# Kernel optimization log

Measured on AMD Instinct MI355X. Metric: run time of the kernel, lower is better.

The kernel has to match this reference:

```python
import jax, jax.numpy as jnp
import numpy as np

N = 1024      # num_features
H = 256       # num_hidden_features
E = 64        # embedding_size
HD = 64       # hidden_size
B = 8192


def setup_inputs() -> dict:
    key = jax.random.key(0)
    ks = jax.random.split(key, 7)
    glorot_e = (2.0 / (N + E)) ** 0.5
    glorot_w = (2.0 / (2 * E + HD)) ** 0.5
    glorot_u = (2.0 / (HD + 1)) ** 0.5
    return {
        "values": jax.random.uniform(ks[0], (B, N), dtype=jnp.float32),
        "feat_emb": jax.random.normal(ks[1], (N, E), dtype=jnp.float32) * glorot_e,
        "hid_emb": jax.random.normal(ks[2], (H, E), dtype=jnp.float32) * glorot_e,
        "W_w": jax.random.normal(ks[3], (2 * E, HD), dtype=jnp.float32) * glorot_w,
        "b_w": jnp.zeros((HD,), dtype=jnp.float32),
        "W_u": jax.random.normal(ks[4], (HD, 1), dtype=jnp.float32) * glorot_u,
        "mask": jax.random.bernoulli(ks[5], 0.5, (N, N + H)),
    }


def _forward(values, feat_emb, hid_emb, W_w, b_w, W_u, mask):
    # full embedding table over extended vocab: [M, E], M = N + H
    full = jnp.concatenate([feat_emb, hid_emb], axis=0)
    # Dense w applied to concat([feat_i, full_j]) == split-matmul, avoids [N,M,2E]
    W1, W2 = W_w[:E], W_w[E:]                      # each [E, HD]
    a = feat_emb @ W1                              # [N, HD]
    b = full @ W2                                  # [M, HD]
    h = jnp.tanh(a[:, None, :] + b[None, :, :] + b_w)  # [N, M, HD]
    score = jnp.squeeze(h @ W_u, axis=-1)          # [N, M]
    score = jnp.where(mask, jnp.exp(score), 0.0)
    score_sum = jnp.sum(score, axis=1, keepdims=True)
    score_sum = jnp.where(score_sum == 0, 1.0, score_sum)
    attention_weights = score / score_sum          # [N, M]
    context = attention_weights @ full             # [N, E]
    return values @ context                        # [B, E]


def reference(values, feat_emb, hid_emb, W_w, b_w, W_u, mask):
    return _forward(values, feat_emb, hid_emb, W_w, b_w, W_u, mask)
```

## Files before the change

### kernel.cpp

```cpp
#include <hip/hip_runtime.h>
#include <hip/hip_bf16.h>

#define NF   1024
#define NHID 256
#define NJ   1280
#define ED   64
#define BATCH 8192

#define K2E   2.8853900817779268f
#define LOG2E 1.4426950408889634f

__device__ __forceinline__ float exp2_fast(float x) {
    float r;
    asm volatile("v_exp_f32 %0, %1" : "=v"(r) : "v"(x));
    return r;
}

__global__ __launch_bounds__(256) void prep_kernel(
    const float* __restrict__ feat, const float* __restrict__ hid,
    const float* __restrict__ Ww, const float* __restrict__ bw,
    float* __restrict__ Ap, float* __restrict__ BvT)
{
    __shared__ __align__(16) float in_s[64][64];
    __shared__ __align__(16) float tout[64][65];
    const int tid = threadIdx.x;
    const int b   = blockIdx.x;
    const bool isA = (b < 16);
    const int e  = tid & 63;
    const int wv = tid >> 6;

    const float* W = isA ? Ww : (Ww + 4096);
    float wcol[64];
    #pragma unroll
    for (int k = 0; k < 64; k++) wcol[k] = W[k * 64 + e];
    const float bias = isA ? 0.f : bw[e];

    const int bb = isA ? b : (b - 16);
    const float* src = isA ? (feat + (size_t)bb * 4096)
                     : (bb < 16 ? (feat + (size_t)bb * 4096)
                                : (hid + (size_t)(bb - 16) * 4096));
    #pragma unroll
    for (int s = 0; s < 4; s++)
        ((float4*)&in_s[0][0])[tid + s * 256] = ((const float4*)src)[tid + s * 256];
    __syncthreads();

    float acc[16];
    #pragma unroll
    for (int r = 0; r < 16; r++) acc[r] = bias;
    for (int k4 = 0; k4 < 64; k4 += 4) {
        #pragma unroll
        for (int r = 0; r < 16; r++) {
            float4 iv = *(const float4*)&in_s[wv * 16 + r][k4];
            acc[r] += iv.x*wcol[k4+0] + iv.y*wcol[k4+1] + iv.z*wcol[k4+2] + iv.w*wcol[k4+3];
        }
    }

    if (isA) {
        #pragma unroll
        for (int r = 0; r < 16; r++)
            Ap[(size_t)(b * 64 + wv * 16 + r) * 64 + e] = acc[r] * K2E;
    } else {
        #pragma unroll
        for (int r = 0; r < 16; r++) tout[wv * 16 + r][e] = acc[r] * K2E;
        __syncthreads();
        const int j0 = bb * 64;
        #pragma unroll
        for (int q = 0; q < 4; q++) {
            float4 v;
            v.x = tout[wv * 16 + q * 4 + 0][e];
            v.y = tout[wv * 16 + q * 4 + 1][e];
            v.z = tout[wv * 16 + q * 4 + 2][e];
            v.w = tout[wv * 16 + q * 4 + 3][e];
            *(float4*)&BvT[(size_t)e * NJ + j0 + wv * 16 + q * 4] = v;
        }
    }
}

__global__ __launch_bounds__(256) void score_kernel(
    const float* __restrict__ Wu, const float* __restrict__ Ap,
    const float* __restrict__ BvT, const void* __restrict__ maskp,
    float* __restrict__ sc)
{
    __shared__ __align__(16) float4 sA4[64];
    __shared__ float sWu2[64];
    __shared__ float sSwuL;
    __shared__ int   mtype_s;

    const int tid = threadIdx.x;
    const int iq  = blockIdx.x / 5;
    const int jc  = blockIdx.x - iq * 5;
    const int i0  = iq * 4;
    const int j   = jc * 256 + tid;

    if (tid < 64) {
        const unsigned int* mw = (const unsigned int*)maskp;
        unsigned int w = mw[tid];
        unsigned long long notf = __ballot(w != 0u && w != 0x3F800000u);
        unsigned long long gt1  = __ballot(w > 1u);
        if (tid == 0) mtype_s = (notf == 0ull) ? 2 : ((gt1 == 0ull) ? 1 : 0);
        float wu = Wu[tid];
        float4 p;
        p.x = Ap[(size_t)(i0 + 0) * 64 + tid];
        p.y = Ap[(size_t)(i0 + 1) * 64 + tid];
        p.z = Ap[(size_t)(i0 + 2) * 64 + tid];
        p.w = Ap[(size_t)(i0 + 3) * 64 + tid];
        sA4[tid]  = p;
        sWu2[tid] = wu * (2.0f * LOG2E);
        float s = wu;
        #pragma unroll
        for (int off = 32; off > 0; off >>= 1) s += __shfl_down(s, off);
        if (tid == 0) sSwuL = s * LOG2E;
    }
    __syncthreads();

    const float* bp = BvT + j;
    float acc0 = 0.f, acc1 = 0.f, acc2 = 0.f, acc3 = 0.f;
    #pragma unroll 8
    for (int e = 0; e < 64; e++) {
        float b  = bp[(size_t)e * NJ];
        float4 a = sA4[e];
        float w2 = sWu2[e];
        float t, r;
        t = a.x + b; r = __builtin_amdgcn_rcpf(exp2_fast(t) + 1.f); acc0 = fmaf(w2, r, acc0);
        t = a.y + b; r = __builtin_amdgcn_rcpf(exp2_fast(t) + 1.f); acc1 = fmaf(w2, r, acc1);
        t = a.z + b; r = __builtin_amdgcn_rcpf(exp2_fast(t) + 1.f); acc2 = fmaf(w2, r, acc2);
        t = a.w + b; r = __builtin_amdgcn_rcpf(exp2_fast(t) + 1.f); acc3 = fmaf(w2, r, acc3);
    }

    const float SwuL = sSwuL;
    const int mtype = mtype_s;
    const unsigned char* m8  = (const unsigned char*)maskp;
    const unsigned int*  m32 = (const unsigned int*)maskp;
    const float*         mfl = (const float*)maskp;
    float av[4] = {acc0, acc1, acc2, acc3};
    #pragma unroll
    for (int i = 0; i < 4; i++) {
        size_t off = (size_t)(i0 + i) * NJ + j;
        bool bm;
        if (mtype == 0)      bm = m8[off]  != 0;
        else if (mtype == 1) bm = m32[off] != 0u;
        else                 bm = mfl[off] != 0.f;
        sc[off] = bm ? exp2_fast(SwuL - av[i]) : 0.f;
    }
}

__global__ __launch_bounds__(256) void ctx_kernel(
    const float* __restrict__ feat, const float* __restrict__ hid,
    const float* __restrict__ sc, float* __restrict__ ctx)
{
    __shared__ __align__(16) float sc_s[4][NJ];
    __shared__ __align__(16) float red[4][16][64];
    __shared__ float ssum_s[4];
    const int tid = threadIdx.x;
    const int i0  = blockIdx.x * 4;

    #pragma unroll
    for (int rep = 0; rep < 5; rep++) {
        int idx = tid + rep * 256;
        int i   = idx / 320;
        int jq  = idx - i * 320;
        *(float4*)&sc_s[i][jq * 4] = *(const float4*)&sc[(size_t)(i0 + i) * NJ + jq * 4];
    }
    __syncthreads();
    {
        int i = tid >> 6, e = tid & 63;
        float s = 0.f;
        #pragma unroll
        for (int g = 0; g < 20; g++) s += sc_s[i][e + g * 64];
        #pragma unroll
        for (int off = 32; off > 0; off >>= 1) s += __shfl_down(s, off);
        if (e == 0) ssum_s[i] = (s == 0.f) ? 1.f : s;
    }

    const int jg = tid >> 4;
    const int e4 = (tid & 15) * 4;
    float4 c[4];
    #pragma unroll
    for (int i = 0; i < 4; i++) c[i] = make_float4(0.f, 0.f, 0.f, 0.f);
    for (int it = 0; it < 80; it++) {
        int j = it * 16 + jg;
        const float* fr = (j < NF) ? (feat + (size_t)j * 64)
                                   : (hid  + (size_t)(j - NF) * 64);
        float4 f = *(const float4*)(fr + e4);
        #pragma unroll
        for (int i = 0; i < 4; i++) {
            float w = sc_s[i][j];
            c[i].x += w*f.x; c[i].y += w*f.y; c[i].z += w*f.z; c[i].w += w*f.w;
        }
    }
    #pragma unroll
    for (int i = 0; i < 4; i++) *(float4*)&red[i][jg][e4] = c[i];
    __syncthreads();
    {
        int half = tid >> 6, e = tid & 63;
        float v = 0.f;
        #pragma unroll
        for (int g = 0; g < 16; g++) v += red[half][g][e];
        ctx[(size_t)(i0 + half) * 64 + e] = v / ssum_s[half];
    }
}

__global__ __launch_bounds__(256) void out_mm_kernel(
    const float* __restrict__ values, const float* __restrict__ ctxp,
    float* __restrict__ dst, int atomic_mode)
{
    __shared__ __align__(16) float vsT[64 * 64];
    __shared__ __align__(16) float cs[64][64];
    const int tid = threadIdx.x;
    const int rt  = blockIdx.x >> 3;
    const int kq  = blockIdx.x & 7;
    const int r0  = rt * 64;
    const int tr  = tid >> 4;
    const int tc4 = (tid & 15) * 4;

    float acc[4][4];
    #pragma unroll
    for (int a = 0; a < 4; a++)
        #pragma unroll
        for (int b = 0; b < 4; b++) acc[a][b] = 0.f;

    for (int ch = 0; ch < 2; ch++) {
        const int k0 = kq * 128 + ch * 64;
        __syncthreads();
        #pragma unroll
        for (int s = 0; s < 4; s++) {
            int t   = tid + s * 256;
            int r   = t >> 4;
            int kk4 = (t & 15) * 4;
            float4 g = *(const float4*)&values[(size_t)(r0 + r) * NF + k0 + kk4];
            int p  = (((r >> 2) + (t & 15)) & 15) * 4 + (r & 3);
            vsT[(kk4 + 0) * 64 + p] = g.x;
            vsT[(kk4 + 1) * 64 + p] = g.y;
            vsT[(kk4 + 2) * 64 + p] = g.z;
            vsT[(kk4 + 3) * 64 + p] = g.w;
        }
        #pragma unroll
        for (int s = 0; s < 4; s++) {
            int t  = tid + s * 256;
            int kk = t >> 4;
            int c4 = (t & 15) * 4;
            *(float4*)&cs[kk][c4] = *(const float4*)&ctxp[(size_t)(k0 + kk) * ED + c4];
        }
        __syncthreads();
        #pragma unroll 8
        for (int k = 0; k < 64; k++) {
            float4 av = *(const float4*)&vsT[k * 64 + (((tr + (k >> 2)) & 15) << 2)];
            float4 bv = *(const float4*)&cs[k][tc4];
            acc[0][0] += av.x*bv.x; acc[0][1] += av.x*bv.y; acc[0][2] += av.x*bv.z; acc[0][3] += av.x*bv.w;
            acc[1][0] += av.y*bv.x; acc[1][1] += av.y*bv.y; acc[1][2] += av.y*bv.z; acc[1][3] += av.y*bv.w;
            acc[2][0] += av.z*bv.x; acc[2][1] += av.z*bv.y; acc[2][2] += av.z*bv.z; acc[2][3] += av.z*bv.w;
            acc[3][0] += av.w*bv.x; acc[3][1] += av.w*bv.y; acc[3][2] += av.w*bv.z; acc[3][3] += av.w*bv.w;
        }
    }
    if (atomic_mode) {
        #pragma unroll
        for (int i2 = 0; i2 < 4; i2++) {
            int r = r0 + tr * 4 + i2;
            float* op = dst + (size_t)r * ED + tc4;
            unsafeAtomicAdd(op + 0, acc[i2][0]);
            unsafeAtomicAdd(op + 1, acc[i2][1]);
            unsafeAtomicAdd(op + 2, acc[i2][2]);
            unsafeAtomicAdd(op + 3, acc[i2][3]);
        }
    } else {
        #pragma unroll
        for (int i2 = 0; i2 < 4; i2++) {
            int r = r0 + tr * 4 + i2;
            float* op = dst + ((size_t)kq * BATCH + r) * ED + tc4;
            *(float4*)op = make_float4(acc[i2][0], acc[i2][1], acc[i2][2], acc[i2][3]);
        }
    }
}

__global__ __launch_bounds__(256) void reduce8_kernel(
    const float* __restrict__ part, float* __restrict__ out)
{
    const size_t S = (size_t)BATCH * ED / 4;
    size_t idx = (size_t)blockIdx.x * 256 + threadIdx.x;
    const float4* p = (const float4*)part;
    float4 r = {0.f, 0.f, 0.f, 0.f};
    #pragma unroll
    for (int q = 0; q < 8; q++) {
        float4 a = p[idx + (size_t)q * S];
        r.x += a.x; r.y += a.y; r.z += a.z; r.w += a.w;
    }
    ((float4*)out)[idx] = r;
}

extern "C" void kernel_launch(void* const* d_in, const int* in_sizes, int n_in,
                              void* d_out, int out_size, void* d_ws, size_t ws_size,
                              hipStream_t stream) {
    const float* values = (const float*)d_in[0];
    const float* feat   = (const float*)d_in[1];
    const float* hid    = (const float*)d_in[2];
    const float* Ww     = (const float*)d_in[3];
    const float* bw     = (const float*)d_in[4];
    const float* Wu     = (const float*)d_in[5];
    const void*  mask   = d_in[6];
    float* out = (float*)d_out;

    float* Ap  = (float*)d_ws;
    float* BvT = Ap + (size_t)NF * 64;
    float* ctx = BvT + (size_t)ED * NJ;
    float* sc  = ctx + (size_t)NF * 64;
    float* part = sc + (size_t)NF * NJ;
    const size_t need = ((size_t)NF*64 + (size_t)ED*NJ + (size_t)NF*64
                         + (size_t)NF*NJ + (size_t)8*BATCH*ED) * sizeof(float);
    const bool wsmode = ws_size >= need;

    hipLaunchKernelGGL(prep_kernel, dim3(36), dim3(256), 0, stream,
                       feat, hid, Ww, bw, Ap, BvT);
    hipLaunchKernelGGL(score_kernel, dim3(1280), dim3(256), 0, stream,
                       Wu, Ap, BvT, mask, sc);
    hipLaunchKernelGGL(ctx_kernel, dim3(256), dim3(256), 0, stream,
                       feat, hid, sc, ctx);
    if (wsmode) {
        hipLaunchKernelGGL(out_mm_kernel, dim3(1024), dim3(256), 0, stream,
                           values, ctx, part, 0);
        hipLaunchKernelGGL(reduce8_kernel, dim3(BATCH * ED / 4 / 256), dim3(256), 0, stream,
                           part, out);
    } else {
        hipMemsetAsync(d_out, 0, (size_t)BATCH * ED * sizeof(float), stream);
        hipLaunchKernelGGL(out_mm_kernel, dim3(1024), dim3(256), 0, stream,
                           values, ctx, out, 1);
    }
}
```

Before: 153.6 us.

## Move Wu reduction to prep, read A/Wu from global in score, halve ctx rows per block

Computes the Wu sum once in prep_kernel and stores it in workspace. score_kernel drops its shared-memory staging of A rows and scaled Wu, reading them directly from global/scalar memory (wave-uniform loads), and folds the 2*log2e scale into a final fma. ctx_kernel now handles 2 rows per block with 512 blocks for more parallelism, at the cost of reloading feature rows twice as often. The asm volatile on v_exp is relaxed to let the compiler schedule it.

```diff
diff --git a/kernel.cpp b/kernel.cpp
--- a/kernel.cpp
+++ b/kernel.cpp
@@ -12,14 +12,15 @@
 
 __device__ __forceinline__ float exp2_fast(float x) {
     float r;
-    asm volatile("v_exp_f32 %0, %1" : "=v"(r) : "v"(x));
+    asm("v_exp_f32 %0, %1" : "=v"(r) : "v"(x));
     return r;
 }
 
 __global__ __launch_bounds__(256) void prep_kernel(
     const float* __restrict__ feat, const float* __restrict__ hid,
     const float* __restrict__ Ww, const float* __restrict__ bw,
-    float* __restrict__ Ap, float* __restrict__ BvT)
+    const float* __restrict__ Wu,
+    float* __restrict__ Ap, float* __restrict__ BvT, float* __restrict__ swu)
 {
     __shared__ __align__(16) float in_s[64][64];
     __shared__ __align__(16) float tout[64][65];
@@ -29,6 +30,13 @@
     const int e  = tid & 63;
     const int wv = tid >> 6;
 
+    if (b == 0 && tid < 64) {
+        float s = Wu[tid];
+        #pragma unroll
+        for (int off = 32; off > 0; off >>= 1) s += __shfl_down(s, off);
+        if (tid == 0) swu[0] = s * LOG2E;
+    }
+
     const float* W = isA ? Ww : (Ww + 4096);
     float wcol[64];
     #pragma unroll
@@ -78,14 +86,10 @@
 
 __global__ __launch_bounds__(256) void score_kernel(
     const float* __restrict__ Wu, const float* __restrict__ Ap,
-    const float* __restrict__ BvT, const void* __restrict__ maskp,
-    float* __restrict__ sc)
-{
-    __shared__ __align__(16) float4 sA4[64];
-    __shared__ float sWu2[64];
-    __shared__ float sSwuL;
-    __shared__ int   mtype_s;
-
+    const float* __restrict__ BvT, const float* __restrict__ swu,
+    const void* __restrict__ maskp, float* __restrict__ sc)
+{
+    __shared__ int mtype_s;
     const int tid = threadIdx.x;
     const int iq  = blockIdx.x / 5;
     const int jc  = blockIdx.x - iq * 5;
@@ -98,36 +102,28 @@
         unsigned long long notf = __ballot(w != 0u && w != 0x3F800000u);
         unsigned long long gt1  = __ballot(w > 1u);
         if (tid == 0) mtype_s = (notf == 0ull) ? 2 : ((gt1 == 0ull) ? 1 : 0);
-        float wu = Wu[tid];
-        float4 p;
-        p.x = Ap[(size_t)(i0 + 0) * 64 + tid];
-        p.y = Ap[(size_t)(i0 + 1) * 64 + tid];
-        p.z = Ap[(size_t)(i0 + 2) * 64 + tid];
-        p.w = Ap[(size_t)(i0 + 3) * 64 + tid];
-        sA4[tid]  = p;
-        sWu2[tid] = wu * (2.0f * LOG2E);
-        float s = wu;
-        #pragma unroll
-        for (int off = 32; off > 0; off >>= 1) s += __shfl_down(s, off);
-        if (tid == 0) sSwuL = s * LOG2E;
     }
     __syncthreads();
 
-    const float* bp = BvT + j;
+    const float* a0p = Ap + (size_t)(i0 + 0) * 64;
+    const float* a1p = Ap + (size_t)(i0 + 1) * 64;
+    const float* a2p = Ap + (size_t)(i0 + 2) * 64;
+    const float* a3p = Ap + (size_t)(i0 + 3) * 64;
+    const float* bp  = BvT + j;
+
     float acc0 = 0.f, acc1 = 0.f, acc2 = 0.f, acc3 = 0.f;
     #pragma unroll 8
     for (int e = 0; e < 64; e++) {
         float b  = bp[(size_t)e * NJ];
-        float4 a = sA4[e];
-        float w2 = sWu2[e];
+        float wu = Wu[e];
         float t, r;
-        t = a.x + b; r = __builtin_amdgcn_rcpf(exp2_fast(t) + 1.f); acc0 = fmaf(w2, r, acc0);
-        t = a.y + b; r = __builtin_amdgcn_rcpf(exp2_fast(t) + 1.f); acc1 = fmaf(w2, r, acc1);
-        t = a.z + b; r = __builtin_amdgcn_rcpf(exp2_fast(t) + 1.f); acc2 = fmaf(w2, r, acc2);
-        t = a.w + b; r = __builtin_amdgcn_rcpf(exp2_fast(t) + 1.f); acc3 = fmaf(w2, r, acc3);
-    }
-
-    const float SwuL = sSwuL;
+        t = a0p[e] + b; r = __builtin_amdgcn_rcpf(exp2_fast(t) + 1.f); acc0 = fmaf(wu, r, acc0);
+        t = a1p[e] + b; r = __builtin_amdgcn_rcpf(exp2_fast(t) + 1.f); acc1 = fmaf(wu, r, acc1);
+        t = a2p[e] + b; r = __builtin_amdgcn_rcpf(exp2_fast(t) + 1.f); acc2 = fmaf(wu, r, acc2);
+        t = a3p[e] + b; r = __builtin_amdgcn_rcpf(exp2_fast(t) + 1.f); acc3 = fmaf(wu, r, acc3);
+    }
+
+    const float SwuL = swu[0];
     const int mtype = mtype_s;
     const unsigned char* m8  = (const unsigned char*)maskp;
     const unsigned int*  m32 = (const unsigned int*)maskp;
@@ -140,7 +136,7 @@
         if (mtype == 0)      bm = m8[off]  != 0;
         else if (mtype == 1) bm = m32[off] != 0u;
         else                 bm = mfl[off] != 0.f;
-        sc[off] = bm ? exp2_fast(SwuL - av[i]) : 0.f;
+        sc[off] = bm ? exp2_fast(fmaf(-K2E, av[i], SwuL)) : 0.f;
     }
 }
 
@@ -148,21 +144,23 @@
     const float* __restrict__ feat, const float* __restrict__ hid,
     const float* __restrict__ sc, float* __restrict__ ctx)
 {
-    __shared__ __align__(16) float sc_s[4][NJ];
-    __shared__ __align__(16) float red[4][16][64];
-    __shared__ float ssum_s[4];
+    __shared__ __align__(16) float sc_s[2][NJ];
+    __shared__ __align__(16) float red[2][16][64];
+    __shared__ float ssum_s[2];
     const int tid = threadIdx.x;
-    const int i0  = blockIdx.x * 4;
-
-    #pragma unroll
-    for (int rep = 0; rep < 5; rep++) {
+    const int i0  = blockIdx.x * 2;
+
+    #pragma unroll
+    for (int rep = 0; rep < 3; rep++) {
         int idx = tid + rep * 256;
-        int i   = idx / 320;
-        int jq  = idx - i * 320;
-        *(float4*)&sc_s[i][jq * 4] = *(const float4*)&sc[(size_t)(i0 + i) * NJ + jq * 4];
+        if (idx < 640) {
+            int i  = idx / 320;
+            int jq = idx - i * 320;
+            *(float4*)&sc_s[i][jq * 4] = *(const float4*)&sc[(size_t)(i0 + i) * NJ + jq * 4];
+        }
     }
     __syncthreads();
-    {
+    if (tid < 128) {
         int i = tid >> 6, e = tid & 63;
         float s = 0.f;
         #pragma unroll
@@ -174,24 +172,20 @@
 
     const int jg = tid >> 4;
     const int e4 = (tid & 15) * 4;
-    float4 c[4];
-    #pragma unroll
-    for (int i = 0; i < 4; i++) c[i] = make_float4(0.f, 0.f, 0.f, 0.f);
+    float4 c0 = {0.f,0.f,0.f,0.f}, c1 = {0.f,0.f,0.f,0.f};
     for (int it = 0; it < 80; it++) {
         int j = it * 16 + jg;
         const float* fr = (j < NF) ? (feat + (size_t)j * 64)
                                    : (hid  + (size_t)(j - NF) * 64);
         float4 f = *(const float4*)(fr + e4);
-        #pragma unroll
-        for (int i = 0; i < 4; i++) {
-            float w = sc_s[i][j];
-            c[i].x += w*f.x; c[i].y += w*f.y; c[i].z += w*f.z; c[i].w += w*f.w;
-        }
-    }
-    #pragma unroll
-    for (int i = 0; i < 4; i++) *(float4*)&red[i][jg][e4] = c[i];
+        float w0 = sc_s[0][j], w1 = sc_s[1][j];
+        c0.x += w0*f.x; c0.y += w0*f.y; c0.z += w0*f.z; c0.w += w0*f.w;
+        c1.x += w1*f.x; c1.y += w1*f.y; c1.z += w1*f.z; c1.w += w1*f.w;
+    }
+    *(float4*)&red[0][jg][e4] = c0;
+    *(float4*)&red[1][jg][e4] = c1;
     __syncthreads();
-    {
+    if (tid < 128) {
         int half = tid >> 6, e = tid & 63;
         float v = 0.f;
         #pragma unroll
@@ -299,20 +293,21 @@
     const void*  mask   = d_in[6];
     float* out = (float*)d_out;
 
-    float* Ap  = (float*)d_ws;
-    float* BvT = Ap + (size_t)NF * 64;
-    float* ctx = BvT + (size_t)ED * NJ;
-    float* sc  = ctx + (size_t)NF * 64;
+    float* Ap   = (float*)d_ws;
+    float* BvT  = Ap + (size_t)NF * 64;
+    float* ctx  = BvT + (size_t)ED * NJ;
+    float* swu  = ctx + (size_t)NF * 64;
+    float* sc   = swu + 64;
     float* part = sc + (size_t)NF * NJ;
-    const size_t need = ((size_t)NF*64 + (size_t)ED*NJ + (size_t)NF*64
+    const size_t need = ((size_t)NF*64 + (size_t)ED*NJ + (size_t)NF*64 + 64
                          + (size_t)NF*NJ + (size_t)8*BATCH*ED) * sizeof(float);
     const bool wsmode = ws_size >= need;
 
     hipLaunchKernelGGL(prep_kernel, dim3(36), dim3(256), 0, stream,
-                       feat, hid, Ww, bw, Ap, BvT);
+                       feat, hid, Ww, bw, Wu, Ap, BvT, swu);
     hipLaunchKernelGGL(score_kernel, dim3(1280), dim3(256), 0, stream,
-                       Wu, Ap, BvT, mask, sc);
-    hipLaunchKernelGGL(ctx_kernel, dim3(256), dim3(256), 0, stream,
+                       Wu, Ap, BvT, swu, mask, sc);
+    hipLaunchKernelGGL(ctx_kernel, dim3(512), dim3(256), 0, stream,
                        feat, hid, sc, ctx);
     if (wsmode) {
         hipLaunchKernelGGL(out_mm_kernel, dim3(1024), dim3(256), 0, stream,
```

After: 146.1 us. -4.9%, faster.
